# Optimization experiments

Measured on AMD Instinct MI355X. Metric: run time of the kernel, lower is better.

## Reference

```python
import jax, jax.numpy as jnp
import numpy as np

C = 100000
D = 512
KEEP_RATIO = 0.5
EPS = 1.1920929e-07  # torch.finfo(float32).eps
K = max(1, int(C * KEEP_RATIO))


def _l2norm(x):
    # F.normalize(dim=-1): x / max(||x||, eps)
    n = jnp.linalg.norm(x, axis=-1, keepdims=True)
    return x / jnp.maximum(n, EPS)


def setup_inputs() -> dict:
    key = jax.random.key(0)
    k1, k2, k3 = jax.random.split(key, 3)
    tensor = jax.random.normal(k1, (1024, D), dtype=jnp.float32)
    target = jax.random.randint(k2, (1024,), 0, C, dtype=jnp.int32)
    # xavier_normal_ on (C, D): std = sqrt(2 / (C + D))
    std = np.sqrt(2.0 / (C + D)).astype(np.float32)
    weight = jax.random.normal(k3, (C, D), dtype=jnp.float32) * std
    return {"tensor": tensor, "target": target, "weight": weight}


def reference(tensor, target, weight):
    # --- target mining (no-grad in original) ---
    t_n = _l2norm(tensor)            # (B, D)
    w_n = _l2norm(weight)            # (C, D)
    # max over batch of cosine similarity -> per-class score (C,)
    scores = jnp.max(jnp.einsum("bd,cd->bc", t_n, w_n), axis=0)
    # ground-truth classes always kept
    scores = scores.at[target].set(2.0)
    _, topk_idx = jax.lax.top_k(scores, K)
    subsample = jnp.sort(topk_idx)                       # (K,) ascending
    # remap targets into subsampled index space (targets guaranteed present)
    new_target = jnp.searchsorted(subsample, target).astype(jnp.int32)
    # --- head ---
    w_sub = weight[subsample]                            # (K, D) gather
    logits = jnp.einsum("bd,kd->bk", _l2norm(tensor), _l2norm(w_sub))
    return logits, new_target
```

## Files before the change

kernel.cpp:

```cpp
#include <hip/hip_runtime.h>

#define C_CLS 100000
#define D_DIM 512
#define B_ROWS 1024
#define K_KEEP 50000
#define EPS_F 1.1920929e-07f
#define MB_CT 32
#define BAND 2e-3f
#define DELTA 4e-4f
#define RMAX 32768

typedef short v8s __attribute__((ext_vector_type(8)));
typedef float v4f __attribute__((ext_vector_type(4)));

struct Ctrl { unsigned prefix; unsigned need; };

__device__ __forceinline__ unsigned key_of(float f){
  unsigned u = __float_as_uint(f);
  return (u & 0x80000000u) ? ~u : (u | 0x80000000u);
}
__device__ __forceinline__ float key_inv(unsigned k){
  unsigned u = (k & 0x80000000u) ? (k & 0x7FFFFFFFu) : ~k;
  return __uint_as_float(u);
}
__device__ __forceinline__ unsigned short f2bf_rne(float f){
  unsigned u = __float_as_uint(f);
  unsigned r = (u + 0x7FFFu + ((u >> 16) & 1u)) >> 16;
  return (unsigned short)r;
}
__device__ __forceinline__ float bf2f(unsigned short h){
  return __uint_as_float(((unsigned)h) << 16);
}


__global__ __launch_bounds__(64) void norm_t_kernel(const float* __restrict__ t, float* __restrict__ tn,
                                                    unsigned short* __restrict__ tnph, unsigned short* __restrict__ tnpl,
                                                    const int* __restrict__ tgt, unsigned* __restrict__ keys){
  int row = blockIdx.x, lane = threadIdx.x;
  if (lane == 0) atomicMax(&keys[tgt[row]], key_of(2.0f));
  const float4* p = (const float4*)(t + (size_t)row * D_DIM);
  float4 a = p[lane*2+0], b = p[lane*2+1];
  float s = a.x*a.x + a.y*a.y + a.z*a.z + a.w*a.w
          + b.x*b.x + b.y*b.y + b.z*b.z + b.w*b.w;
  #pragma unroll
  for (int off = 32; off; off >>= 1) s += __shfl_xor(s, off);
  float den = fmaxf(sqrtf(s), EPS_F);
  float o[8] = {a.x/den, a.y/den, a.z/den, a.w/den, b.x/den, b.y/den, b.z/den, b.w/den};
  float4* q = (float4*)(tn + (size_t)row * D_DIM);
  q[lane*2+0] = make_float4(o[0],o[1],o[2],o[3]);
  q[lane*2+1] = make_float4(o[4],o[5],o[6],o[7]);
  v8s hv, lv;
  #pragma unroll
  for (int j = 0; j < 8; ++j){
    unsigned short h = f2bf_rne(o[j]);
    hv[j] = (short)h;
    lv[j] = (short)f2bf_rne(o[j] - bf2f(h));
  }
  size_t di = (size_t)((row & ~15) + (lane >> 2)) * 512 + (lane & 3) * 128 + (row & 15) * 8;
  *(v8s*)(tnph + di) = hv;
  *(v8s*)(tnpl + di) = lv;
}

__device__ __forceinline__ void load_a2(const unsigned short* __restrict__ tp, int b0, int ks, int lane, v8s* dst){
  #pragma unroll
  for (int i = 0; i < 2; ++i){
    int t = b0 + i*16 + (ks >> 5);
    dst[i] = *(const v8s*)(tp + (size_t)t * 512 + lane * 8);
  }
}

__global__ __launch_bounds__(512, 8) void mine_kernel(
    const unsigned short* __restrict__ tnph, const unsigned short* __restrict__ tnpl,
    const float* __restrict__ w, unsigned* __restrict__ keys,
    float* __restrict__ S, float* __restrict__ winv_g){
  __shared__ unsigned short lw[MB_CT * D_DIM];
  __shared__ float wn[MB_CT];
  const int tid = threadIdx.x;
  const int lane = tid & 63;
  const int cb = blockIdx.x * MB_CT;
  #pragma unroll
  for (int st = 0; st < 4; ++st){
    int g = tid + st * 512;
    int row = g >> 6, fc = g & 63;
    int c = cb + row; if (c >= C_CLS) c = C_CLS - 1;
    const float4* src = (const float4*)(w + (size_t)c * D_DIM + fc * 8);
    float4 v0 = src[0], v1 = src[1];
    float vv[8] = {v0.x,v0.y,v0.z,v0.w,v1.x,v1.y,v1.z,v1.w};
    float s = 0.f;
    #pragma unroll
    for (int off = 32; off; off >>= 1){}
    s = 0.f;
    #pragma unroll
    for (int j = 0; j < 8; ++j) s += vv[j]*vv[j];
    #pragma unroll
    for (int off = 32; off; off >>= 1) s += __shfl_xor(s, off);
    if (lane == 0) wn[row] = 1.0f / fmaxf(sqrtf(s), EPS_F);
    v8s hv;
    #pragma unroll
    for (int j = 0; j < 8; ++j) hv[j] = (short)f2bf_rne(vv[j]);
    int csw = fc ^ (row & 7);
    *(v8s*)&lw[(size_t)row * D_DIM + csw * 8] = hv;
  }
  __syncthreads();
  if (tid < MB_CT && cb + tid < C_CLS) winv_g[cb + tid] = wn[tid];

  const int wv = tid >> 6;
  const int lr = lane & 15, lg = lane >> 4;
  const int bbase = wv * 128;
  float runmax[2] = {-1e30f,-1e30f};
  v4f acc[2][2];
  #pragma unroll
  for (int j = 0; j < 2; ++j)
    #pragma unroll
    for (int i = 0; i < 2; ++i) acc[j][i] = (v4f){0.f,0.f,0.f,0.f};

  v8s cah[2], cal[2];
  load_a2(tnph, bbase, 0, lane, cah);
  load_a2(tnpl, bbase, 0, lane, cal);

  for (int it = 0; it < 64; ++it){
    const int chunk = it >> 4, ks = (it & 15) << 5;
    const int b0 = bbase + chunk * 32;
    v8s nah[2], nal[2];
    if (it < 63){
      int nit = it + 1;
      int nb0 = bbase + (nit >> 4) * 32, nks = (nit & 15) << 5;
      load_a2(tnph, nb0, nks, lane, nah);
      load_a2(tnpl, nb0, nks, lane, nal);
    }
    v8s bh[2];
    #pragma unroll
    for (int j = 0; j < 2; ++j){
      int row = j*16 + lr;
      int ch = ((ks >> 3) + lg) ^ (lr & 7);
      bh[j] = *(const v8s*)&lw[(size_t)row * D_DIM + ch * 8];
    }
    #pragma unroll
    for (int j = 0; j < 2; ++j)
      #pragma unroll
      for (int i = 0; i < 2; ++i){
        acc[j][i] = __builtin_amdgcn_mfma_f32_16x16x32_bf16(cah[i], bh[j], acc[j][i], 0, 0, 0);
        acc[j][i] = __builtin_amdgcn_mfma_f32_16x16x32_bf16(cal[i], bh[j], acc[j][i], 0, 0, 0);
      }
    if ((it & 15) == 15){
      #pragma unroll
      for (int j = 0; j < 2; ++j){
        float m = acc[j][0][0];
        #pragma unroll
        for (int i = 0; i < 2; ++i)
          #pragma unroll
          for (int r = 0; r < 4; ++r) m = fmaxf(m, acc[j][i][r]);
        runmax[j] = fmaxf(runmax[j], m);
        int cls = cb + j*16 + lr;
        if (cls < C_CLS){
          #pragma unroll
          for (int i = 0; i < 2; ++i){
            float4 v = make_float4(acc[j][i][0], acc[j][i][1], acc[j][i][2], acc[j][i][3]);
            *(float4*)(S + (size_t)cls * B_ROWS + b0 + i*16 + lg*4) = v;
          }
        }
        #pragma unroll
        for (int i = 0; i < 2; ++i) acc[j][i] = (v4f){0.f,0.f,0.f,0.f};
      }
    }
    if (it < 63){
      #pragma unroll
      for (int i = 0; i < 2; ++i){ cah[i] = nah[i]; cal[i] = nal[i]; }
    }
  }
  #pragma unroll
  for (int j = 0; j < 2; ++j){
    float m = runmax[j];
    m = fmaxf(m, __shfl_xor(m, 16));
    m = fmaxf(m, __shfl_xor(m, 32));
    int cls = cb + j*16 + lr;
    if (lg == 0 && cls < C_CLS)
      atomicMax(&keys[cls], key_of(m * wn[j*16 + lr]));
  }
}

__global__ __launch_bounds__(256) void histsel_kernel(const unsigned* __restrict__ keys, unsigned* __restrict__ hist,
                                                      unsigned* __restrict__ done, Ctrl* __restrict__ ctrl, int shift){
  __shared__ unsigned h[256];
  __shared__ int lastf;
  int t = threadIdx.x;
  h[t] = 0u;
  __syncthreads();
  unsigned himask = (shift >= 24) ? 0u : (0xFFFFFFFFu << (shift + 8));
  unsigned prefix = (shift == 24) ? 0u : (ctrl->prefix & himask);
  for (int c = blockIdx.x * 256 + t; c < C_CLS; c += gridDim.x * 256){
    unsigned k = keys[c];
    if ((k & himask) == prefix) atomicAdd(&h[(k >> shift) & 255], 1u);
  }
  __syncthreads();
  if (h[t]) atomicAdd(&hist[t], h[t]);
  __threadfence();
  if (t == 0) lastf = (atomicAdd(done, 1u) == (unsigned)(gridDim.x - 1));
  __syncthreads();
  if (lastf){
    unsigned v = __hip_atomic_load(&hist[t], __ATOMIC_RELAXED, __HIP_MEMORY_SCOPE_AGENT);
    h[t] = v;
    __syncthreads();
    if (t == 0){
      unsigned need = (shift == 24) ? (unsigned)K_KEEP : ctrl->need;
      unsigned pfx  = (shift == 24) ? 0u : ctrl->prefix;
      unsigned cum = 0; int b;
      for (b = 255; b >= 0; --b){
        if (cum + h[b] >= need) break;
        cum += h[b];
      }
      if (b < 0) b = 0;
      ctrl->prefix = pfx | ((unsigned)b << shift);
      ctrl->need = need - cum;
      __hip_atomic_store(done, 0u, __ATOMIC_RELAXED, __HIP_MEMORY_SCOPE_AGENT);
    }
    __hip_atomic_store(&hist[t], 0u, __ATOMIC_RELAXED, __HIP_MEMORY_SCOPE_AGENT);
  }
}

__global__ void band_kernel(const unsigned* __restrict__ keys, const Ctrl* __restrict__ ctrl,
                            int* __restrict__ rlist, int* __restrict__ rcount){
  int c = blockIdx.x * 256 + threadIdx.x;
  if (c >= C_CLS) return;
  unsigned k = keys[c];
  if (k == key_of(2.0f)) return;
  float t = key_inv(ctrl->prefix);
  if (fabsf(key_inv(k) - t) <= BAND){
    int i = atomicAdd(rcount, 1);
    if (i < RMAX) rlist[i] = c;
  }
}

__global__ __launch_bounds__(256) void refine_kernel(
    const float* __restrict__ tn, const float* __restrict__ w,
    const float* __restrict__ winv, const float* __restrict__ S,
    const int* __restrict__ rlist, const int* __restrict__ rcount,
    unsigned* __restrict__ keys){
  __shared__ float red[256];
  __shared__ double dred[256];
  __shared__ int cand[32];
  __shared__ int ncand;
  int n = *rcount; if (n > RMAX) n = RMAX;
  int t = threadIdx.x;
  for (int i = blockIdx.x; i < n; i += gridDim.x){
    int c = rlist[i];
    const v4f* srow = (const v4f*)(S + (size_t)c * B_ROWS);
    v4f sv = srow[t];
    float m = fmaxf(fmaxf(sv[0],sv[1]), fmaxf(sv[2],sv[3]));
    red[t] = m; __syncthreads();
    for (int off2 = 128; off2; off2 >>= 1){
      if (t < off2) red[t] = fmaxf(red[t], red[t+off2]);
      __syncthreads();
    }
    float thr = red[0] - DELTA;
    if (t == 0) ncand = 0;
    __syncthreads();
    #pragma unroll
    for (int e = 0; e < 4; ++e){
      if (sv[e] >= thr){
        int ci = atomicAdd(&ncand, 1);
        if (ci < 32) cand[ci] = t*4 + e;
      }
    }
    __syncthreads();
    int nc = ncand; if (nc > 32) nc = 32;
    const float* wrow = w + (size_t)c * D_DIM;
    double w0 = (double)wrow[2*t], w1 = (double)wrow[2*t+1];
    double best = -1e300;
    for (int q = 0; q < nc; ++q){
      int b = cand[q];
      const float* tr = tn + (size_t)b * D_DIM;
      double p = fma((double)tr[2*t], w0, (double)tr[2*t+1] * w1);
      dred[t] = p; __syncthreads();
      for (int off2 = 128; off2; off2 >>= 1){
        if (t < off2) dred[t] += dred[t+off2];
        __syncthreads();
      }
      if (t == 0) best = fmax(best, dred[0]);
      __syncthreads();
    }
    if (t == 0) keys[c] = key_of((float)(best * (double)winv[c]));
    __syncthreads();
  }
}

__global__ __launch_bounds__(256) void scanA_kernel(const unsigned* __restrict__ keys, const Ctrl* __restrict__ ctrl,
                                                    uint2* __restrict__ bsum2, unsigned* __restrict__ done2, int nb){
  __shared__ unsigned red[256];
  __shared__ int lastf;
  int t = threadIdx.x;
  unsigned T = ctrl->prefix;
  int base = blockIdx.x * 1024 + t * 4;
  unsigned pack = 0;
  #pragma unroll
  for (int j = 0; j < 4; ++j){
    int c = base + j;
    if (c < C_CLS){
      unsigned k = keys[c];
      if (k > T) pack += 0x10000u;
      else if (k == T) pack += 1u;
    }
  }
  red[t] = pack; __syncthreads();
  for (int off = 128; off; off >>= 1){
    if (t < off) red[t] += red[t + off];
    __syncthreads();
  }
  if (t == 0) bsum2[blockIdx.x] = make_uint2(red[0] >> 16, red[0] & 0xFFFFu);
  __threadfence();
  if (t == 0) lastf = (atomicAdd(done2, 1u) == (unsigned)(gridDim.x - 1));
  __syncthreads();
  if (lastf && t == 0){
    unsigned rg = 0, re = 0;
    for (int i = 0; i < nb; ++i){
      unsigned vx = __hip_atomic_load(&bsum2[i].x, __ATOMIC_RELAXED, __HIP_MEMORY_SCOPE_AGENT);
      unsigned vy = __hip_atomic_load(&bsum2[i].y, __ATOMIC_RELAXED, __HIP_MEMORY_SCOPE_AGENT);
      __hip_atomic_store(&bsum2[i].x, rg, __ATOMIC_RELAXED, __HIP_MEMORY_SCOPE_AGENT);
      __hip_atomic_store(&bsum2[i].y, re, __ATOMIC_RELAXED, __HIP_MEMORY_SCOPE_AGENT);
      rg += vx; re += vy;
    }
    __hip_atomic_store(done2, 0u, __ATOMIC_RELAXED, __HIP_MEMORY_SCOPE_AGENT);
  }
}

__global__ __launch_bounds__(256) void scanC_kernel(const unsigned* __restrict__ keys, const Ctrl* __restrict__ ctrl,
                                                    const uint2* __restrict__ bsum2, unsigned* __restrict__ pos,
                                                    int* __restrict__ sel){
  __shared__ unsigned ls[256];
  int t = threadIdx.x;
  unsigned T = ctrl->prefix, need = ctrl->need;
  int base = blockIdx.x * 1024 + t * 4;
  unsigned gtv[4], eqv[4], pack = 0;
  #pragma unroll
  for (int j = 0; j < 4; ++j){
    int c = base + j;
    unsigned k = (c < C_CLS) ? keys[c] : 0u;
    gtv[j] = (c < C_CLS && k > T) ? 1u : 0u;
    eqv[j] = (c < C_CLS && k == T) ? 1u : 0u;
    pack += (gtv[j] << 16) + eqv[j];
  }
  ls[t] = pack; __syncthreads();
  for (int off = 1; off < 256; off <<= 1){
    unsigned v = (t >= off) ? ls[t - off] : 0u;
    __syncthreads();
    ls[t] += v;
    __syncthreads();
  }
  unsigned excl = ls[t] - pack;
  uint2 bs = bsum2[blockIdx.x];
  unsigned gtx = bs.x + (excl >> 16);
  unsigned eqx = bs.y + (excl & 0xFFFFu);
  #pragma unroll
  for (int j = 0; j < 4; ++j){
    int c = base + j;
    if (c < C_CLS){
      unsigned p = gtx + (eqx < need ? eqx : need);
      pos[c] = p;
      if (gtv[j] || (eqv[j] && eqx < need)) sel[p] = c;
      gtx += gtv[j]; eqx += eqv[j];
    }
  }
}

__global__ void ntgt_kernel(const int* __restrict__ tgt, const unsigned* __restrict__ pos, float* __restrict__ out){
  int b = blockIdx.x * 256 + threadIdx.x;
  if (b < B_ROWS) out[(size_t)B_ROWS * K_KEEP + b] = (float)pos[tgt[b]];
}

__global__ __launch_bounds__(256) void head_copy_kernel(const float* __restrict__ S, const float* __restrict__ winv,
                                                        const int* __restrict__ sel, float* __restrict__ out){
  __shared__ float tile[64][68];
  __shared__ float wsc[64];
  int k0 = blockIdx.y * 64;
  int b0 = blockIdx.x * 64;
  int tid = threadIdx.x;
  int nk = K_KEEP - k0; if (nk > 64) nk = 64;
  if (tid < 64){
    int kk = k0 + tid;
    wsc[tid] = (kk < K_KEEP) ? winv[sel[kk]] : 0.f;
  }
  int r = tid >> 4, lq = tid & 15;
  #pragma unroll
  for (int itr = 0; itr < 4; ++itr){
    int i = itr * 16 + r;
    if (i < nk){
      int c = sel[k0 + i];
      float4 v = *(const float4*)(S + (size_t)c * B_ROWS + b0 + lq * 4);
      *(float4*)&tile[i][lq * 4] = v;
    }
  }
  __syncthreads();
  #pragma unroll
  for (int itw = 0; itw < 4; ++itw){
    int bb = itw * 16 + r;
    int kk = lq * 4;
    size_t obase = (size_t)(b0 + bb) * K_KEEP + k0;
    if (kk + 3 < nk){
      float4 v = make_float4(tile[kk+0][bb]*wsc[kk+0], tile[kk+1][bb]*wsc[kk+1],
                             tile[kk+2][bb]*wsc[kk+2], tile[kk+3][bb]*wsc[kk+3]);
      *(float4*)(out + obase + kk) = v;
    } else {
      for (int e = 0; e < 4; ++e)
        if (kk + e < nk) out[obase + kk + e] = tile[kk+e][bb]*wsc[kk+e];
    }
  }
}

extern "C" void kernel_launch(void* const* d_in, const int* in_sizes, int n_in,
                              void* d_out, int out_size, void* d_ws, size_t ws_size,
                              hipStream_t stream){
  const float* tensor = (const float*)d_in[0];
  const int*   target = (const int*)d_in[1];
  const float* weight = (const float*)d_in[2];
  float* out = (float*)d_out;

  char* ws = (char*)d_ws;
  size_t off = 0;
  auto carve = [&](size_t bytes) -> char* {
    char* p = ws + off;
    off = (off + bytes + 511) & ~(size_t)511;
    return p;
  };
  float*          tn   = (float*)carve((size_t)B_ROWS * D_DIM * 4);
  unsigned short* tnph = (unsigned short*)carve((size_t)B_ROWS * D_DIM * 2);
  unsigned short* tnpl = (unsigned short*)carve((size_t)B_ROWS * D_DIM * 2);
  float*          winv = (float*)carve((size_t)C_CLS * 4);
  size_t zs = off;
  unsigned* keys   = (unsigned*)carve((size_t)C_CLS * 4);
  unsigned* hist   = (unsigned*)carve(256 * 4);
  unsigned* done   = (unsigned*)carve(64);
  unsigned* done2  = (unsigned*)carve(64);
  int*      rcount = (int*)carve(64);
  size_t ze = off;
  Ctrl*     ctrl   = (Ctrl*)carve(64);
  uint2*    bsum2  = (uint2*)carve(128 * 8);
  int*      rlist  = (int*)carve((size_t)RMAX * 4);
  unsigned* pos    = (unsigned*)carve((size_t)C_CLS * 4);
  int*      sel    = (int*)carve((size_t)K_KEEP * 4);
  float*    S      = (float*)carve((size_t)C_CLS * B_ROWS * 4);
  (void)in_sizes; (void)n_in; (void)out_size; (void)ws_size;

  hipMemsetAsync(ws + zs, 0, ze - zs, stream);

  norm_t_kernel<<<B_ROWS, 64, 0, stream>>>(tensor, tn, tnph, tnpl, target, keys);

  mine_kernel<<<(C_CLS + MB_CT - 1) / MB_CT, 512, 0, stream>>>(tnph, tnpl, weight, keys, S, winv);

  for (int shift = 24; shift >= 0; shift -= 8)
    histsel_kernel<<<128, 256, 0, stream>>>(keys, hist, done, ctrl, shift);

  band_kernel<<<(C_CLS + 255) / 256, 256, 0, stream>>>(keys, ctrl, rlist, rcount);
  refine_kernel<<<2048, 256, 0, stream>>>(tn, weight, winv, S, rlist, rcount, keys);

  for (int shift = 24; shift >= 0; shift -= 8)
    histsel_kernel<<<128, 256, 0, stream>>>(keys, hist, done, ctrl, shift);

  const int nb = (C_CLS + 1023) / 1024;
  scanA_kernel<<<nb, 256, 0, stream>>>(keys, ctrl, bsum2, done2, nb);
  scanC_kernel<<<nb, 256, 0, stream>>>(keys, ctrl, bsum2, pos, sel);

  ntgt_kernel<<<(B_ROWS + 255) / 256, 256, 0, stream>>>(target, pos, out);
  head_copy_kernel<<<dim3(B_ROWS / 64, (K_KEEP + 63) / 64), 256, 0, stream>>>(S, winv, sel, out);
}
```

Before: 722.3 us.

## Double class tile per block in mining kernel with new LDS tile layout

The mining kernel now processes 64 classes per block instead of 32, so each loaded A fragment of the normalized batch feeds twice as many MFMAs. It also replaces the row-XOR LDS swizzle with a per-16x32 tile layout in which each lane's B fragment is read contiguously. The aim is to cut reloads of the batch operand from global memory and to reduce LDS bank conflicts. In exchange the block uses more LDS and more accumulator registers, the launch-bound occupancy hint drops from 8 to 4, and there are half as many blocks.

```diff
diff --git a/kernel.cpp b/kernel.cpp
--- a/kernel.cpp
+++ b/kernel.cpp
@@ -5,7 +5,7 @@
 #define B_ROWS 1024
 #define K_KEEP 50000
 #define EPS_F 1.1920929e-07f
-#define MB_CT 32
+#define MB_CT 64
 #define BAND 2e-3f
 #define DELTA 4e-4f
 #define RMAX 32768
@@ -69,7 +69,7 @@
   }
 }
 
-__global__ __launch_bounds__(512, 8) void mine_kernel(
+__global__ __launch_bounds__(512, 4) void mine_kernel(
     const unsigned short* __restrict__ tnph, const unsigned short* __restrict__ tnpl,
     const float* __restrict__ w, unsigned* __restrict__ keys,
     float* __restrict__ S, float* __restrict__ winv_g){
@@ -79,7 +79,7 @@
   const int lane = tid & 63;
   const int cb = blockIdx.x * MB_CT;
   #pragma unroll
-  for (int st = 0; st < 4; ++st){
+  for (int st = 0; st < 8; ++st){
     int g = tid + st * 512;
     int row = g >> 6, fc = g & 63;
     int c = cb + row; if (c >= C_CLS) c = C_CLS - 1;
@@ -88,9 +88,6 @@
     float vv[8] = {v0.x,v0.y,v0.z,v0.w,v1.x,v1.y,v1.z,v1.w};
     float s = 0.f;
     #pragma unroll
-    for (int off = 32; off; off >>= 1){}
-    s = 0.f;
-    #pragma unroll
     for (int j = 0; j < 8; ++j) s += vv[j]*vv[j];
     #pragma unroll
     for (int off = 32; off; off >>= 1) s += __shfl_xor(s, off);
@@ -98,8 +95,11 @@
     v8s hv;
     #pragma unroll
     for (int j = 0; j < 8; ++j) hv[j] = (short)f2bf_rne(vv[j]);
-    int csw = fc ^ (row & 7);
-    *(v8s*)&lw[(size_t)row * D_DIM + csw * 8] = hv;
+    int t = (row >> 4) * 16 + (fc >> 2);
+    int kslot = fc & 3;
+    int m = ((fc >> 2) & 1) * 4 + kslot;
+    int a16 = t * 64 + kslot * 16 + ((row & 15) ^ m);
+    *(v8s*)&lw[(size_t)a16 * 8] = hv;
   }
   __syncthreads();
   if (tid < MB_CT && cb + tid < C_CLS) winv_g[cb + tid] = wn[tid];
@@ -107,10 +107,10 @@
   const int wv = tid >> 6;
   const int lr = lane & 15, lg = lane >> 4;
   const int bbase = wv * 128;
-  float runmax[2] = {-1e30f,-1e30f};
-  v4f acc[2][2];
-  #pragma unroll
-  for (int j = 0; j < 2; ++j)
+  float runmax[4] = {-1e30f,-1e30f,-1e30f,-1e30f};
+  v4f acc[4][2];
+  #pragma unroll
+  for (int j = 0; j < 4; ++j)
     #pragma unroll
     for (int i = 0; i < 2; ++i) acc[j][i] = (v4f){0.f,0.f,0.f,0.f};
 
@@ -119,7 +119,7 @@
   load_a2(tnpl, bbase, 0, lane, cal);
 
   for (int it = 0; it < 64; ++it){
-    const int chunk = it >> 4, ks = (it & 15) << 5;
+    const int chunk = it >> 4, kt = it & 15;
     const int b0 = bbase + chunk * 32;
     v8s nah[2], nal[2];
     if (it < 63){
@@ -128,15 +128,19 @@
       load_a2(tnph, nb0, nks, lane, nah);
       load_a2(tnpl, nb0, nks, lane, nal);
     }
-    v8s bh[2];
-    #pragma unroll
-    for (int j = 0; j < 2; ++j){
-      int row = j*16 + lr;
-      int ch = ((ks >> 3) + lg) ^ (lr & 7);
-      bh[j] = *(const v8s*)&lw[(size_t)row * D_DIM + ch * 8];
-    }
-    #pragma unroll
-    for (int j = 0; j < 2; ++j)
+    v8s bh[4];
+    {
+      int m = (kt & 1) * 4 + lg;
+      int ci = (lr ^ m);
+      #pragma unroll
+      for (int j = 0; j < 4; ++j){
+        int t = j * 16 + kt;
+        int a16 = t * 64 + lg * 16 + ci;
+        bh[j] = *(const v8s*)&lw[(size_t)a16 * 8];
+      }
+    }
+    #pragma unroll
+    for (int j = 0; j < 4; ++j)
       #pragma unroll
       for (int i = 0; i < 2; ++i){
         acc[j][i] = __builtin_amdgcn_mfma_f32_16x16x32_bf16(cah[i], bh[j], acc[j][i], 0, 0, 0);
@@ -144,13 +148,13 @@
       }
     if ((it & 15) == 15){
       #pragma unroll
-      for (int j = 0; j < 2; ++j){
-        float m = acc[j][0][0];
+      for (int j = 0; j < 4; ++j){
+        float mm = acc[j][0][0];
         #pragma unroll
         for (int i = 0; i < 2; ++i)
           #pragma unroll
-          for (int r = 0; r < 4; ++r) m = fmaxf(m, acc[j][i][r]);
-        runmax[j] = fmaxf(runmax[j], m);
+          for (int r = 0; r < 4; ++r) mm = fmaxf(mm, acc[j][i][r]);
+        runmax[j] = fmaxf(runmax[j], mm);
         int cls = cb + j*16 + lr;
         if (cls < C_CLS){
           #pragma unroll
@@ -169,7 +173,7 @@
     }
   }
   #pragma unroll
-  for (int j = 0; j < 2; ++j){
+  for (int j = 0; j < 4; ++j){
     float m = runmax[j];
     m = fmaxf(m, __shfl_xor(m, 16));
     m = fmaxf(m, __shfl_xor(m, 32));
```

Result: faster. 614.5 us (median of 3 runs) (-14.9%).
